# Performance work log

Measured on AMD Instinct MI355X. Metric: run time of the kernel, lower is better.

## Reference

```python
import jax, jax.numpy as jnp
import numpy as np

UNITS = 512
BACKCAST_LEN = 512
FORECAST_LEN = 128
NB_HARMONICS = 64  # forecast_length // 2
THETAS_DIM = 2 * NB_HARMONICS
BATCH = 16384


def _seasonality_basis(length, nb_harmonics):
    # t = 2*pi*arange(L)/L ; rows interleaved [cos(0*t), sin(0*t), cos(1*t), sin(1*t), ...]
    t = 2.0 * np.pi * jnp.arange(length, dtype=jnp.float32) / length
    i = jnp.arange(nb_harmonics, dtype=jnp.float32)[:, None]  # [H,1]
    angles = i * t[None, :]                                   # [H,L]
    basis = jnp.stack([jnp.cos(angles), jnp.sin(angles)], axis=1)  # [H,2,L]
    return basis.reshape(2 * nb_harmonics, length)            # [2H,L]


def setup_inputs() -> dict:
    key = jax.random.key(0)
    ks = jax.random.split(key, 10)
    s_in = 1.0 / np.sqrt(BACKCAST_LEN)
    s_u = 1.0 / np.sqrt(UNITS)
    return {
        "x": jax.random.normal(ks[0], (BATCH, BACKCAST_LEN), jnp.float32),
        "W1": jax.random.normal(ks[1], (UNITS, BACKCAST_LEN), jnp.float32) * s_in,
        "b1": jax.random.normal(ks[2], (UNITS,), jnp.float32) * s_in,
        "W2": jax.random.normal(ks[3], (UNITS, UNITS), jnp.float32) * s_u,
        "b2": jax.random.normal(ks[4], (UNITS,), jnp.float32) * s_u,
        "W3": jax.random.normal(ks[5], (UNITS, UNITS), jnp.float32) * s_u,
        "b3": jax.random.normal(ks[6], (UNITS,), jnp.float32) * s_u,
        "W4": jax.random.normal(ks[7], (UNITS, UNITS), jnp.float32) * s_u,
        "b4": jax.random.normal(ks[8], (UNITS,), jnp.float32) * s_u,
        "Wt": jax.random.normal(ks[9], (THETAS_DIM, UNITS), jnp.float32) * s_u,
    }


def reference(x, W1, b1, W2, b2, W3, b3, W4, b4, Wt):
    h = jax.nn.relu(x @ W1.T + b1)
    h = jax.nn.relu(h @ W2.T + b2)
    h = jax.nn.relu(h @ W3.T + b3)
    h = jax.nn.relu(h @ W4.T + b4)
    theta = h @ Wt.T  # [B, 2H], shared thetas (share_thetas=True)
    basis_b = _seasonality_basis(BACKCAST_LEN, NB_HARMONICS)  # [2H, Lb]
    basis_f = _seasonality_basis(FORECAST_LEN, NB_HARMONICS)  # [2H, Lf]
    backcast = theta @ basis_b  # [B, Lb]
    forecast = theta @ basis_f  # [B, Lf]
    return (backcast, forecast)
```

## Files before the change

### kernel.cpp

```cpp
#include <hip/hip_runtime.h>
#include <hip/hip_bf16.h>
#include <math.h>


#define BATCH 16384
#define ROWS  64

typedef __bf16 bf16x8 __attribute__((ext_vector_type(8)));
typedef float  f32x4  __attribute__((ext_vector_type(4)));

__device__ __forceinline__ unsigned short f2bf(float f) {
  union { float f; unsigned u; } v; v.f = f;
  unsigned r = v.u + 0x7fff + ((v.u >> 16) & 1);
  return (unsigned short)(r >> 16);
}

__global__ __launch_bounds__(256) void prep_kernel(
    const float* __restrict__ W1, const float* __restrict__ W2,
    const float* __restrict__ W3, const float* __restrict__ W4,
    const float* __restrict__ Wt,
    unsigned short* __restrict__ W1p, unsigned short* __restrict__ W2p,
    unsigned short* __restrict__ W3p, unsigned short* __restrict__ W4p,
    unsigned short* __restrict__ Wtp,
    unsigned short* __restrict__ basp) {
  const int t = blockIdx.x * 256 + threadIdx.x;
  if (t < 139264) {
    const float* src; unsigned short* dst; int u;
    if (t < 131072) {
      const int w = t >> 15; u = t & 32767;
      src = (w == 0) ? W1 : (w == 1) ? W2 : (w == 2) ? W3 : W4;
      dst = (w == 0) ? W1p : (w == 1) ? W2p : (w == 2) ? W3p : W4p;
    } else {
      u = t - 131072; src = Wt; dst = Wtp;
    }
    const int lane = u & 63, ks = (u >> 6) & 15, cf = u >> 10;
    const int col = cf * 16 + (lane & 15);
    const int k0  = ks * 32 + (lane >> 4) * 8;
    const float4* s = (const float4*)(src + (size_t)col * 512 + k0);
    const float4 a = s[0], b = s[1];
    uint4 o;
    o.x = f2bf(a.x) | ((unsigned)f2bf(a.y) << 16);
    o.y = f2bf(a.z) | ((unsigned)f2bf(a.w) << 16);
    o.z = f2bf(b.x) | ((unsigned)f2bf(b.y) << 16);
    o.w = f2bf(b.z) | ((unsigned)f2bf(b.w) << 16);
    ((uint4*)dst)[u] = o;
  } else if (t < 149504) {
    const int u = t - 139264;
    const int lane = u & 63, ks = (u >> 6) & 3, cf = u >> 8;
    const int col = cf * 16 + (lane & 15);
    const int r0  = ks * 32 + (lane >> 4) * 8;
    int l, L;
    if (col < 512) { l = col; L = 512; } else { l = col - 512; L = 128; }
    const float w0 = 6.283185307179586f * (float)l / (float)L;
    unsigned short e[8];
#pragma unroll
    for (int i = 0; i < 8; ++i) {
      const int r = r0 + i;
      const float ang = (float)(r >> 1) * w0;
      e[i] = f2bf((r & 1) ? sinf(ang) : cosf(ang));
    }
    uint4 o;
    o.x = e[0] | ((unsigned)e[1] << 16);
    o.y = e[2] | ((unsigned)e[3] << 16);
    o.z = e[4] | ((unsigned)e[5] << 16);
    o.w = e[6] | ((unsigned)e[7] << 16);
    ((uint4*)basp)[u] = o;
  }
}

__device__ __forceinline__ void wait_lds_and_barrier() {
  asm volatile("s_waitcnt lgkmcnt(0)" ::: "memory");
  __builtin_amdgcn_sched_barrier(0);
  __builtin_amdgcn_s_barrier();
  __builtin_amdgcn_sched_barrier(0);
}

template <int PHASE, bool PF_NEXT>
__device__ __forceinline__ void layer512(
    const unsigned short* hin, unsigned short* hout,
    const bf16x8* __restrict__ wcur, const bf16x8* __restrict__ wnext,
    const float* __restrict__ bias, bf16x8 (&bv)[3][4],
    const int wv, const int lane) {
  const int l15 = lane & 15, g = lane >> 4;
  f32x4 acc[4][4];
#pragma unroll
  for (int m = 0; m < 4; ++m)
#pragma unroll
    for (int n = 0; n < 4; ++n) acc[m][n] = (f32x4){0.f, 0.f, 0.f, 0.f};

  int rb[4], am[4];
#pragma unroll
  for (int m = 0; m < 4; ++m) {
    const int row = m * 16 + l15;
    rb[m] = row * 1024;
    am[m] = (row & 7) << 4;
  }

#pragma unroll
  for (int ks = 0; ks < 16; ++ks) {
    if (ks < 14) {
#pragma unroll
      for (int n = 0; n < 4; ++n)
        bv[(PHASE + ks + 2) % 3][n] = wcur[n * 1024 + (ks + 2) * 64];
    } else if (PF_NEXT) {
#pragma unroll
      for (int n = 0; n < 4; ++n)
        bv[(PHASE + ks + 2) % 3][n] = wnext[n * 1024 + (ks - 14) * 64];
    }
    bf16x8 av[4];
    const int kb = ks * 64 + g * 16;
#pragma unroll
    for (int m = 0; m < 4; ++m)
      av[m] = *(const bf16x8*)((const char*)hin + rb[m] + (kb ^ am[m]));
    __builtin_amdgcn_s_setprio(1);
#pragma unroll
    for (int m = 0; m < 4; ++m)
#pragma unroll
      for (int n = 0; n < 4; ++n)
        acc[m][n] = __builtin_amdgcn_mfma_f32_16x16x32_bf16(
            bv[(PHASE + ks) % 3][n], av[m], acc[m][n], 0, 0, 0);
    __builtin_amdgcn_s_setprio(0);
  }

  float4 bias4[4];
#pragma unroll
  for (int n = 0; n < 4; ++n)
    bias4[n] = *(const float4*)(bias + wv * 64 + n * 16 + g * 4);
#pragma unroll
  for (int m = 0; m < 4; ++m) {
    const int row = m * 16 + l15;
    const int sw  = (row & 7) << 4;
#pragma unroll
    for (int n = 0; n < 4; ++n) {
      const float v0 = fmaxf(acc[m][n][0] + bias4[n].x, 0.f);
      const float v1 = fmaxf(acc[m][n][1] + bias4[n].y, 0.f);
      const float v2 = fmaxf(acc[m][n][2] + bias4[n].z, 0.f);
      const float v3 = fmaxf(acc[m][n][3] + bias4[n].w, 0.f);
      uint2 o;
      o.x = f2bf(v0) | ((unsigned)f2bf(v1) << 16);
      o.y = f2bf(v2) | ((unsigned)f2bf(v3) << 16);
      const int c0 = (wv * 64 + n * 16 + g * 4) * 2;
      *(uint2*)((char*)hout + row * 1024 + (c0 ^ sw)) = o;
    }
  }
  wait_lds_and_barrier();
}

__global__ __launch_bounds__(512, 2) void fused_nbeats(
    const float* __restrict__ x,
    const bf16x8* __restrict__ W1p, const float* __restrict__ b1,
    const bf16x8* __restrict__ W2p, const float* __restrict__ b2,
    const bf16x8* __restrict__ W3p, const float* __restrict__ b3,
    const bf16x8* __restrict__ W4p, const float* __restrict__ b4,
    const bf16x8* __restrict__ Wtp,
    const bf16x8* __restrict__ basp,
    float* __restrict__ out) {
  __shared__ __align__(16) unsigned short h0[ROWS * 512];
  __shared__ __align__(16) unsigned short h1[ROWS * 512];

  const int tid  = threadIdx.x;
  const int lane = tid & 63;
  const int wv   = tid >> 6;
  const int l15  = lane & 15, g = lane >> 4;
  const int r0   = blockIdx.x * ROWS;

  const bf16x8* w1 = W1p + (size_t)wv * 4096 + lane;
  const bf16x8* w2 = W2p + (size_t)wv * 4096 + lane;
  const bf16x8* w3 = W3p + (size_t)wv * 4096 + lane;
  const bf16x8* w4 = W4p + (size_t)wv * 4096 + lane;

  bf16x8 bv[3][4];
#pragma unroll
  for (int s = 0; s < 2; ++s)
#pragma unroll
    for (int n = 0; n < 4; ++n) bv[s][n] = w1[n * 1024 + s * 64];

  {
    const float4* xs = (const float4*)(x + (size_t)r0 * 512);
#pragma unroll
    for (int j = 0; j < 16; ++j) {
      const int f = tid + j * 512;
      const int row = f >> 7, c4 = f & 127;
      const float4 v = xs[f];
      uint2 o;
      o.x = f2bf(v.x) | ((unsigned)f2bf(v.y) << 16);
      o.y = f2bf(v.z) | ((unsigned)f2bf(v.w) << 16);
      *(uint2*)((char*)h0 + row * 1024 + ((c4 * 8) ^ ((row & 7) << 4))) = o;
    }
  }
  wait_lds_and_barrier();

  layer512<0, true >(h0, h1, w1, w2, b1, bv, wv, lane);
  layer512<1, true >(h1, h0, w2, w3, b2, bv, wv, lane);
  layer512<2, true >(h0, h1, w3, w4, b3, bv, wv, lane);
  layer512<0, false>(h1, h0, w4, (const bf16x8*)0, b4, bv, wv, lane);

  {
    const bf16x8* tb = Wtp + (size_t)wv * 1024 + lane;
    bf16x8 tv[4];
#pragma unroll
    for (int s = 0; s < 3; ++s) tv[s] = tb[s * 64];

    int rb[4], am[4];
#pragma unroll
    for (int m = 0; m < 4; ++m) {
      const int row = m * 16 + l15;
      rb[m] = row * 1024;
      am[m] = (row & 7) << 4;
    }
    f32x4 tacc[4];
#pragma unroll
    for (int m = 0; m < 4; ++m) tacc[m] = (f32x4){0.f, 0.f, 0.f, 0.f};
#pragma unroll
    for (int ks = 0; ks < 16; ++ks) {
      if (ks < 13) tv[(ks + 3) & 3] = tb[(ks + 3) * 64];
      bf16x8 av[4];
      const int kb = ks * 64 + g * 16;
#pragma unroll
      for (int m = 0; m < 4; ++m)
        av[m] = *(const bf16x8*)((const char*)h0 + rb[m] + (kb ^ am[m]));
      __builtin_amdgcn_s_setprio(1);
#pragma unroll
      for (int m = 0; m < 4; ++m)
        tacc[m] = __builtin_amdgcn_mfma_f32_16x16x32_bf16(
            tv[ks & 3], av[m], tacc[m], 0, 0, 0);
      __builtin_amdgcn_s_setprio(0);
    }
#pragma unroll
    for (int m = 0; m < 4; ++m) {
      const int row = m * 16 + l15;
      const int sw  = (row & 7) << 4;
      uint2 o;
      o.x = f2bf(tacc[m][0]) | ((unsigned)f2bf(tacc[m][1]) << 16);
      o.y = f2bf(tacc[m][2]) | ((unsigned)f2bf(tacc[m][3]) << 16);
      const int c0 = (wv * 16 + g * 4) * 2;
      *(uint2*)((char*)h1 + row * 256 + (c0 ^ sw)) = o;
    }
  }
  wait_lds_and_barrier();

  {
    const bf16x8* bb = basp + (size_t)wv * 1280 + lane;
    bf16x8 bvv[2][5];
#pragma unroll
    for (int n = 0; n < 5; ++n) bvv[0][n] = bb[n * 256];

    f32x4 facc[4][5];
#pragma unroll
    for (int m = 0; m < 4; ++m)
#pragma unroll
      for (int n = 0; n < 5; ++n) facc[m][n] = (f32x4){0.f, 0.f, 0.f, 0.f};
    int rb2[4], am2[4];
#pragma unroll
    for (int m = 0; m < 4; ++m) {
      const int row = m * 16 + l15;
      rb2[m] = row * 256;
      am2[m] = (row & 7) << 4;
    }
#pragma unroll
    for (int ks = 0; ks < 4; ++ks) {
      if (ks < 3) {
#pragma unroll
        for (int n = 0; n < 5; ++n) bvv[(ks + 1) & 1][n] = bb[n * 256 + (ks + 1) * 64];
      }
      bf16x8 av[4];
      const int kb = ks * 64 + g * 16;
#pragma unroll
      for (int m = 0; m < 4; ++m)
        av[m] = *(const bf16x8*)((const char*)h1 + rb2[m] + (kb ^ am2[m]));
      __builtin_amdgcn_s_setprio(1);
#pragma unroll
      for (int n = 0; n < 5; ++n)
#pragma unroll
        for (int m = 0; m < 4; ++m)
          facc[m][n] = __builtin_amdgcn_mfma_f32_16x16x32_bf16(
              bvv[ks & 1][n], av[m], facc[m][n], 0, 0, 0);
      __builtin_amdgcn_s_setprio(0);
    }
#pragma unroll
    for (int n = 0; n < 5; ++n) {
      const int c0 = wv * 80 + n * 16 + g * 4;
#pragma unroll
      for (int m = 0; m < 4; ++m) {
        const int row = r0 + m * 16 + l15;
        float4 o = make_float4(facc[m][n][0], facc[m][n][1],
                               facc[m][n][2], facc[m][n][3]);
        if (c0 < 512)
          *(float4*)(out + (size_t)row * 512 + c0) = o;
        else
          *(float4*)(out + (size_t)BATCH * 512 + (size_t)row * 128 + (c0 - 512)) = o;
      }
    }
  }
}

extern "C" void kernel_launch(void* const* d_in, const int* in_sizes, int n_in,
                              void* d_out, int out_size, void* d_ws, size_t ws_size,
                              hipStream_t stream) {
  const float* x  = (const float*)d_in[0];
  const float* W1 = (const float*)d_in[1];
  const float* b1 = (const float*)d_in[2];
  const float* W2 = (const float*)d_in[3];
  const float* b2 = (const float*)d_in[4];
  const float* W3 = (const float*)d_in[5];
  const float* b3 = (const float*)d_in[6];
  const float* W4 = (const float*)d_in[7];
  const float* b4 = (const float*)d_in[8];
  const float* Wt = (const float*)d_in[9];

  unsigned short* ws  = (unsigned short*)d_ws;
  unsigned short* W1p = ws;
  unsigned short* W2p = ws + 262144;
  unsigned short* W3p = ws + 524288;
  unsigned short* W4p = ws + 786432;
  unsigned short* Wtp = ws + 1048576;
  unsigned short* basp = ws + 1114112;

  prep_kernel<<<584, 256, 0, stream>>>(W1, W2, W3, W4, Wt,
                                       W1p, W2p, W3p, W4p, Wtp, basp);
  fused_nbeats<<<BATCH / ROWS, 512, 0, stream>>>(
      x, (const bf16x8*)W1p, b1, (const bf16x8*)W2p, b2,
      (const bf16x8*)W3p, b3, (const bf16x8*)W4p, b4,
      (const bf16x8*)Wtp, (const bf16x8*)basp, (float*)d_out);
}
```

Baseline: 140.5 us.

## Stream weight chunks into LDS via async global_load_lds double buffering

Weights for the four hidden layers are now staged through a double-buffered LDS ring using async global-to-LDS copies. The prep kernel reorders packed weights into contiguous 32 KB chunks. A single activation buffer is updated in place, with an extra barrier between the MFMA reads and the epilogue writes. Theta is staged in the freed weight buffer, and setprio hints are removed. This trades per-wave register prefetch of weights for shared staging; it adds LDS traffic and vmcnt waits but frees registers.

```diff
diff --git a/kernel.cpp b/kernel.cpp
--- a/kernel.cpp
+++ b/kernel.cpp
@@ -13,6 +13,26 @@
   union { float f; unsigned u; } v; v.f = f;
   unsigned r = v.u + 0x7fff + ((v.u >> 16) & 1);
   return (unsigned short)(r >> 16);
+}
+
+__device__ __forceinline__ void async_copy16(const void* g, void* l) {
+  __builtin_amdgcn_global_load_lds(
+      (const __attribute__((address_space(1))) unsigned int*)g,
+      (__attribute__((address_space(3))) unsigned int*)l,
+      16, 0, 0);
+}
+
+__device__ __forceinline__ void wait_vmcnt4() {
+  asm volatile("s_waitcnt vmcnt(4)" ::: "memory");
+}
+__device__ __forceinline__ void wait_vmcnt0() {
+  asm volatile("s_waitcnt vmcnt(0)" ::: "memory");
+}
+__device__ __forceinline__ void wait_lds_and_barrier() {
+  asm volatile("s_waitcnt lgkmcnt(0)" ::: "memory");
+  __builtin_amdgcn_sched_barrier(0);
+  __builtin_amdgcn_s_barrier();
+  __builtin_amdgcn_sched_barrier(0);
 }
 
 __global__ __launch_bounds__(256) void prep_kernel(
@@ -24,18 +44,14 @@
     unsigned short* __restrict__ Wtp,
     unsigned short* __restrict__ basp) {
   const int t = blockIdx.x * 256 + threadIdx.x;
-  if (t < 139264) {
-    const float* src; unsigned short* dst; int u;
-    if (t < 131072) {
-      const int w = t >> 15; u = t & 32767;
-      src = (w == 0) ? W1 : (w == 1) ? W2 : (w == 2) ? W3 : W4;
-      dst = (w == 0) ? W1p : (w == 1) ? W2p : (w == 2) ? W3p : W4p;
-    } else {
-      u = t - 131072; src = Wt; dst = Wtp;
-    }
-    const int lane = u & 63, ks = (u >> 6) & 15, cf = u >> 10;
-    const int col = cf * 16 + (lane & 15);
-    const int k0  = ks * 32 + (lane >> 4) * 8;
+  if (t < 131072) {
+    const int w = t >> 15;
+    const int u = t & 32767;
+    const float* src = (w == 0) ? W1 : (w == 1) ? W2 : (w == 2) ? W3 : W4;
+    unsigned short* dst = (w == 0) ? W1p : (w == 1) ? W2p : (w == 2) ? W3p : W4p;
+    const int c = u >> 11, wv = (u >> 8) & 7, n = (u >> 6) & 3, lane = u & 63;
+    const int col = (wv * 4 + n) * 16 + (lane & 15);
+    const int k0  = c * 32 + (lane >> 4) * 8;
     const float4* s = (const float4*)(src + (size_t)col * 512 + k0);
     const float4 a = s[0], b = s[1];
     uint4 o;
@@ -44,6 +60,19 @@
     o.z = f2bf(b.x) | ((unsigned)f2bf(b.y) << 16);
     o.w = f2bf(b.z) | ((unsigned)f2bf(b.w) << 16);
     ((uint4*)dst)[u] = o;
+  } else if (t < 139264) {
+    const int u = t - 131072;
+    const int lane = u & 63, ks = (u >> 6) & 15, cf = u >> 10;
+    const int col = cf * 16 + (lane & 15);
+    const int k0  = ks * 32 + (lane >> 4) * 8;
+    const float4* s = (const float4*)(Wt + (size_t)col * 512 + k0);
+    const float4 a = s[0], b = s[1];
+    uint4 o;
+    o.x = f2bf(a.x) | ((unsigned)f2bf(a.y) << 16);
+    o.y = f2bf(a.z) | ((unsigned)f2bf(a.w) << 16);
+    o.z = f2bf(b.x) | ((unsigned)f2bf(b.y) << 16);
+    o.w = f2bf(b.z) | ((unsigned)f2bf(b.w) << 16);
+    ((uint4*)Wtp)[u] = o;
   } else if (t < 149504) {
     const int u = t - 139264;
     const int lane = u & 63, ks = (u >> 6) & 3, cf = u >> 8;
@@ -68,59 +97,57 @@
   }
 }
 
-__device__ __forceinline__ void wait_lds_and_barrier() {
-  asm volatile("s_waitcnt lgkmcnt(0)" ::: "memory");
-  __builtin_amdgcn_sched_barrier(0);
-  __builtin_amdgcn_s_barrier();
-  __builtin_amdgcn_sched_barrier(0);
-}
-
-template <int PHASE, bool PF_NEXT>
+__device__ __forceinline__ void zero_acc(f32x4 (&acc)[4][4]) {
+#pragma unroll
+  for (int m = 0; m < 4; ++m)
+#pragma unroll
+    for (int n = 0; n < 4; ++n) acc[m][n] = (f32x4){0.f, 0.f, 0.f, 0.f};
+}
+
+template <int L>
 __device__ __forceinline__ void layer512(
-    const unsigned short* hin, unsigned short* hout,
-    const bf16x8* __restrict__ wcur, const bf16x8* __restrict__ wnext,
-    const float* __restrict__ bias, bf16x8 (&bv)[3][4],
-    const int wv, const int lane) {
+    unsigned short* h, unsigned short (*Wc)[16384], const char* Wall,
+    const float* __restrict__ bias,
+    const int wv, const int lane, const int (&rb)[4], const int (&am)[4]) {
   const int l15 = lane & 15, g = lane >> 4;
   f32x4 acc[4][4];
-#pragma unroll
-  for (int m = 0; m < 4; ++m)
-#pragma unroll
-    for (int n = 0; n < 4; ++n) acc[m][n] = (f32x4){0.f, 0.f, 0.f, 0.f};
-
-  int rb[4], am[4];
-#pragma unroll
-  for (int m = 0; m < 4; ++m) {
-    const int row = m * 16 + l15;
-    rb[m] = row * 1024;
-    am[m] = (row & 7) << 4;
-  }
-
-#pragma unroll
-  for (int ks = 0; ks < 16; ++ks) {
-    if (ks < 14) {
-#pragma unroll
-      for (int n = 0; n < 4; ++n)
-        bv[(PHASE + ks + 2) % 3][n] = wcur[n * 1024 + (ks + 2) * 64];
-    } else if (PF_NEXT) {
-#pragma unroll
-      for (int n = 0; n < 4; ++n)
-        bv[(PHASE + ks + 2) % 3][n] = wnext[n * 1024 + (ks - 14) * 64];
-    }
+  zero_acc(acc);
+
+  const int woff = wv * 4096 + lane * 16;
+
+#pragma unroll
+  for (int c = 0; c < 16; ++c) {
+    const int G = L * 16 + c;
+    if (G == 63) wait_vmcnt0(); else wait_vmcnt4();
+
+    bf16x8 wf[4];
+#pragma unroll
+    for (int n = 0; n < 4; ++n)
+      wf[n] = *(const bf16x8*)((const char*)Wc[c & 1] + wv * 4096 + n * 1024 + lane * 16);
     bf16x8 av[4];
-    const int kb = ks * 64 + g * 16;
+    const int kb = c * 64 + g * 16;
 #pragma unroll
     for (int m = 0; m < 4; ++m)
-      av[m] = *(const bf16x8*)((const char*)hin + rb[m] + (kb ^ am[m]));
-    __builtin_amdgcn_s_setprio(1);
+      av[m] = *(const bf16x8*)((const char*)h + rb[m] + (kb ^ am[m]));
 #pragma unroll
     for (int m = 0; m < 4; ++m)
 #pragma unroll
       for (int n = 0; n < 4; ++n)
         acc[m][n] = __builtin_amdgcn_mfma_f32_16x16x32_bf16(
-            bv[(PHASE + ks) % 3][n], av[m], acc[m][n], 0, 0, 0);
-    __builtin_amdgcn_s_setprio(0);
-  }
+            wf[n], av[m], acc[m][n], 0, 0, 0);
+
+    __builtin_amdgcn_sched_barrier(0);
+    if (G + 2 <= 63) {
+      const char* gsrc = Wall + (size_t)(G + 2) * 32768 + woff;
+      char* ldst = (char*)Wc[c & 1] + woff;
+#pragma unroll
+      for (int j = 0; j < 4; ++j)
+        async_copy16(gsrc + j * 1024, ldst + j * 1024);
+    }
+    __builtin_amdgcn_sched_barrier(0);
+  }
+
+  wait_lds_and_barrier();
 
   float4 bias4[4];
 #pragma unroll
@@ -140,7 +167,7 @@
       o.x = f2bf(v0) | ((unsigned)f2bf(v1) << 16);
       o.y = f2bf(v2) | ((unsigned)f2bf(v3) << 16);
       const int c0 = (wv * 64 + n * 16 + g * 4) * 2;
-      *(uint2*)((char*)hout + row * 1024 + (c0 ^ sw)) = o;
+      *(uint2*)((char*)h + row * 1024 + (c0 ^ sw)) = o;
     }
   }
   wait_lds_and_barrier();
@@ -148,32 +175,39 @@
 
 __global__ __launch_bounds__(512, 2) void fused_nbeats(
     const float* __restrict__ x,
-    const bf16x8* __restrict__ W1p, const float* __restrict__ b1,
-    const bf16x8* __restrict__ W2p, const float* __restrict__ b2,
-    const bf16x8* __restrict__ W3p, const float* __restrict__ b3,
-    const bf16x8* __restrict__ W4p, const float* __restrict__ b4,
+    const unsigned short* __restrict__ W1p, const float* __restrict__ b1,
+    const float* __restrict__ b2, const float* __restrict__ b3,
+    const float* __restrict__ b4,
     const bf16x8* __restrict__ Wtp,
     const bf16x8* __restrict__ basp,
     float* __restrict__ out) {
-  __shared__ __align__(16) unsigned short h0[ROWS * 512];
-  __shared__ __align__(16) unsigned short h1[ROWS * 512];
+  __shared__ __align__(16) unsigned short h[ROWS * 512];
+  __shared__ __align__(16) unsigned short Wc[2][16384];
 
   const int tid  = threadIdx.x;
   const int lane = tid & 63;
   const int wv   = tid >> 6;
   const int l15  = lane & 15, g = lane >> 4;
   const int r0   = blockIdx.x * ROWS;
-
-  const bf16x8* w1 = W1p + (size_t)wv * 4096 + lane;
-  const bf16x8* w2 = W2p + (size_t)wv * 4096 + lane;
-  const bf16x8* w3 = W3p + (size_t)wv * 4096 + lane;
-  const bf16x8* w4 = W4p + (size_t)wv * 4096 + lane;
-
-  bf16x8 bv[3][4];
-#pragma unroll
-  for (int s = 0; s < 2; ++s)
-#pragma unroll
-    for (int n = 0; n < 4; ++n) bv[s][n] = w1[n * 1024 + s * 64];
+  const char* Wall = (const char*)W1p;
+
+  int rb[4], am[4];
+#pragma unroll
+  for (int m = 0; m < 4; ++m) {
+    const int row = m * 16 + l15;
+    rb[m] = row * 1024;
+    am[m] = (row & 7) << 4;
+  }
+
+  const int woff = wv * 4096 + lane * 16;
+#pragma unroll
+  for (int G = 0; G < 2; ++G) {
+    const char* gsrc = Wall + (size_t)G * 32768 + woff;
+    char* ldst = (char*)Wc[G & 1] + woff;
+#pragma unroll
+    for (int j = 0; j < 4; ++j)
+      async_copy16(gsrc + j * 1024, ldst + j * 1024);
+  }
 
   {
     const float4* xs = (const float4*)(x + (size_t)r0 * 512);
@@ -185,29 +219,23 @@
       uint2 o;
       o.x = f2bf(v.x) | ((unsigned)f2bf(v.y) << 16);
       o.y = f2bf(v.z) | ((unsigned)f2bf(v.w) << 16);
-      *(uint2*)((char*)h0 + row * 1024 + ((c4 * 8) ^ ((row & 7) << 4))) = o;
+      *(uint2*)((char*)h + row * 1024 + ((c4 * 8) ^ ((row & 7) << 4))) = o;
     }
   }
   wait_lds_and_barrier();
 
-  layer512<0, true >(h0, h1, w1, w2, b1, bv, wv, lane);
-  layer512<1, true >(h1, h0, w2, w3, b2, bv, wv, lane);
-  layer512<2, true >(h0, h1, w3, w4, b3, bv, wv, lane);
-  layer512<0, false>(h1, h0, w4, (const bf16x8*)0, b4, bv, wv, lane);
-
+  layer512<0>(h, Wc, Wall, b1, wv, lane, rb, am);
+  layer512<1>(h, Wc, Wall, b2, wv, lane, rb, am);
+  layer512<2>(h, Wc, Wall, b3, wv, lane, rb, am);
+  layer512<3>(h, Wc, Wall, b4, wv, lane, rb, am);
+
+  unsigned short* thetaL = Wc[0];
   {
     const bf16x8* tb = Wtp + (size_t)wv * 1024 + lane;
     bf16x8 tv[4];
 #pragma unroll
     for (int s = 0; s < 3; ++s) tv[s] = tb[s * 64];
 
-    int rb[4], am[4];
-#pragma unroll
-    for (int m = 0; m < 4; ++m) {
-      const int row = m * 16 + l15;
-      rb[m] = row * 1024;
-      am[m] = (row & 7) << 4;
-    }
     f32x4 tacc[4];
 #pragma unroll
     for (int m = 0; m < 4; ++m) tacc[m] = (f32x4){0.f, 0.f, 0.f, 0.f};
@@ -218,14 +246,13 @@
       const int kb = ks * 64 + g * 16;
 #pragma unroll
       for (int m = 0; m < 4; ++m)
-        av[m] = *(const bf16x8*)((const char*)h0 + rb[m] + (kb ^ am[m]));
-      __builtin_amdgcn_s_setprio(1);
+        av[m] = *(const bf16x8*)((const char*)h + rb[m] + (kb ^ am[m]));
 #pragma unroll
       for (int m = 0; m < 4; ++m)
         tacc[m] = __builtin_amdgcn_mfma_f32_16x16x32_bf16(
             tv[ks & 3], av[m], tacc[m], 0, 0, 0);
-      __builtin_amdgcn_s_setprio(0);
-    }
+    }
+    wait_lds_and_barrier();
 #pragma unroll
     for (int m = 0; m < 4; ++m) {
       const int row = m * 16 + l15;
@@ -234,7 +261,7 @@
       o.x = f2bf(tacc[m][0]) | ((unsigned)f2bf(tacc[m][1]) << 16);
       o.y = f2bf(tacc[m][2]) | ((unsigned)f2bf(tacc[m][3]) << 16);
       const int c0 = (wv * 16 + g * 4) * 2;
-      *(uint2*)((char*)h1 + row * 256 + (c0 ^ sw)) = o;
+      *(uint2*)((char*)thetaL + row * 256 + (c0 ^ sw)) = o;
     }
   }
   wait_lds_and_barrier();
@@ -250,13 +277,9 @@
     for (int m = 0; m < 4; ++m)
 #pragma unroll
       for (int n = 0; n < 5; ++n) facc[m][n] = (f32x4){0.f, 0.f, 0.f, 0.f};
-    int rb2[4], am2[4];
-#pragma unroll
-    for (int m = 0; m < 4; ++m) {
-      const int row = m * 16 + l15;
-      rb2[m] = row * 256;
-      am2[m] = (row & 7) << 4;
-    }
+    int rb2[4];
+#pragma unroll
+    for (int m = 0; m < 4; ++m) rb2[m] = (m * 16 + l15) * 256;
 #pragma unroll
     for (int ks = 0; ks < 4; ++ks) {
       if (ks < 3) {
@@ -267,15 +290,13 @@
       const int kb = ks * 64 + g * 16;
 #pragma unroll
       for (int m = 0; m < 4; ++m)
-        av[m] = *(const bf16x8*)((const char*)h1 + rb2[m] + (kb ^ am2[m]));
-      __builtin_amdgcn_s_setprio(1);
+        av[m] = *(const bf16x8*)((const char*)thetaL + rb2[m] + (kb ^ am[m]));
 #pragma unroll
       for (int n = 0; n < 5; ++n)
 #pragma unroll
         for (int m = 0; m < 4; ++m)
           facc[m][n] = __builtin_amdgcn_mfma_f32_16x16x32_bf16(
               bvv[ks & 1][n], av[m], facc[m][n], 0, 0, 0);
-      __builtin_amdgcn_s_setprio(0);
     }
 #pragma unroll
     for (int n = 0; n < 5; ++n) {
@@ -319,7 +340,6 @@
   prep_kernel<<<584, 256, 0, stream>>>(W1, W2, W3, W4, Wt,
                                        W1p, W2p, W3p, W4p, Wtp, basp);
   fused_nbeats<<<BATCH / ROWS, 512, 0, stream>>>(
-      x, (const bf16x8*)W1p, b1, (const bf16x8*)W2p, b2,
-      (const bf16x8*)W3p, b3, (const bf16x8*)W4p, b4,
+      x, W1p, b1, b2, b3, b4,
       (const bf16x8*)Wtp, (const bf16x8*)basp, (float*)d_out);
 }
```

Result: slower. 146.8 us (+4.5%).
